# Performance work log

Measured on AMD Instinct MI355X. Metric: run time of the kernel, lower is better.

The kernel has to match this reference:

```python
import jax, jax.numpy as jnp
import numpy as np

B, T, D = 512, 128, 768
CD, SD, P = 192, 128, 128
FEAT = CD + SD + 1  # 321
LN_EPS = 1e-5


def setup_inputs() -> dict:
    key = jax.random.key(0)
    ks = jax.random.split(key, 10)
    return {
        'H': jax.random.normal(ks[0], (B, T, D), jnp.float32),
        'tt': jax.random.randint(ks[1], (B, T), 0, 2, jnp.int64),
        'attn': jnp.ones((B, T), jnp.int64),
        'Wc': jax.random.normal(ks[2], (CD, 2 * D), jnp.float32) * 0.02,
        'bc': jax.random.normal(ks[3], (CD,), jnp.float32) * 0.02,
        'Ws': jax.random.normal(ks[4], (SD, 2 * D), jnp.float32) * 0.02,
        'bs': jax.random.normal(ks[5], (SD,), jnp.float32) * 0.02,
        'gate': jnp.array([0.5], jnp.float32),
        'ln_g': jnp.ones((FEAT,), jnp.float32),
        'ln_b': jnp.zeros((FEAT,), jnp.float32),
        'Wcls': jax.random.normal(ks[6], (2, FEAT), jnp.float32) * 0.02,
        'bcls': jax.random.normal(ks[7], (2,), jnp.float32) * 0.02,
        'dirs': jax.random.normal(ks[8], (P, D), jnp.float32),
    }


def reference(H, tt, attn, Wc, bc, Ws, bs, gate, ln_g, ln_b, Wcls, bcls, dirs):
    dt = H.dtype
    cls = H[:, 0]                                   # [B, D]
    mask0 = (tt == 0) & (attn == 1)                 # [B, T]
    mask1 = (tt == 1) & (attn == 1)

    def mmean(mask):
        mf = mask.astype(dt)
        s = jnp.einsum('btd,bt->bd', H, mf)
        cnt = jnp.maximum(mask.sum(1, keepdims=True), 1).astype(dt)
        return s / cnt

    rep = jnp.concatenate([cls, mmean(mask0) - mmean(mask1)], axis=1)  # [B, 2D]
    C = rep @ Wc.T + bc
    S = rep @ Ws.T + bs
    g = jax.nn.sigmoid(gate)                        # [1]
    fused = jnp.concatenate([C * (1 - g), S * g], axis=1)  # [B, CD+SD]

    # batched max-sliced W1: project, push masked tokens to +inf, sort along T
    dirs_n = dirs / jnp.linalg.norm(dirs, axis=1, keepdims=True)
    proj = jnp.einsum('btd,pd->btp', H, dirs_n)     # [B, T, P]
    inf = jnp.asarray(jnp.inf, dt)
    xp = jnp.sort(jnp.where(mask0[:, :, None], proj, inf), axis=1)
    yp = jnp.sort(jnp.where(mask1[:, :, None], proj, inf), axis=1)
    n0 = mask0.sum(1)
    n1 = mask1.sum(1)
    mm = jnp.minimum(n0, n1)                        # [B] ragged truncation length
    valid = (jnp.arange(T)[None, :] < mm[:, None])[:, :, None]  # [B, T, 1]
    xs = jnp.where(valid, xp, 0.0)
    ys = jnp.where(valid, yp, 0.0)
    diff = jnp.abs(xs - ys).sum(1) / jnp.maximum(mm, 1)[:, None].astype(dt)  # [B, P]
    d_ot = diff.max(1, keepdims=True)               # [B, 1]

    feat = jnp.concatenate([fused, d_ot], axis=1)   # [B, 321]
    mu = feat.mean(-1, keepdims=True)
    var = feat.var(-1, keepdims=True)
    normed = (feat - mu) / jnp.sqrt(var + LN_EPS) * ln_g + ln_b
    logits = normed @ Wcls.T + bcls                 # [B, 2]

    ortho = jnp.mean((Wc @ Ws.T) ** 2)
    return logits, ortho
```

## Files before the change

kernel.cpp:

```cpp
#include <hip/hip_runtime.h>
#include <hip/hip_bf16.h>

constexpr int B_ = 512;
constexpr int T_ = 128;
constexpr int D_ = 768;
constexpr int CD_ = 192;
constexpr int SD_ = 128;
constexpr int P_ = 128;
constexpr int FEAT_ = 321;
constexpr float LN_EPS_ = 1e-5f;

constexpr size_t REP_SZ   = (size_t)B_ * 2 * D_;
constexpr size_t DN16_FLT = (size_t)P_ * D_ / 2;

typedef __attribute__((ext_vector_type(8))) short short8;
typedef __attribute__((ext_vector_type(4))) float f32x4;

__device__ __forceinline__ unsigned short f2bf(float x) {
    unsigned u = __float_as_uint(x);
    return (unsigned short)((u + 0x7FFFu + ((u >> 16) & 1u)) >> 16);
}
__device__ __forceinline__ float bf2f(unsigned short h) {
    return __uint_as_float((unsigned)h << 16);
}

__global__ __launch_bounds__(256) void k_dirs(const float* __restrict__ dirs,
                                              unsigned short* __restrict__ dn16) {
    int p = blockIdx.x;
    int tid = threadIdx.x;
    float s = 0.f;
    for (int d = tid; d < D_; d += 256) {
        float v = dirs[(size_t)p * D_ + d];
        s = fmaf(v, v, s);
    }
    __shared__ float red[256];
    red[tid] = s;
    __syncthreads();
    for (int off = 128; off > 0; off >>= 1) {
        if (tid < off) red[tid] += red[tid + off];
        __syncthreads();
    }
    float inv = 1.0f / sqrtf(red[0]);
    for (int d = tid; d < D_; d += 256) {
        dn16[(size_t)p * D_ + d] = f2bf(dirs[(size_t)p * D_ + d] * inv);
    }
}

constexpr int NIT_ = 24;
constexpr int BUF_U16_ = 8192;
constexpr int HT_STR_ = 136;

__global__ __launch_bounds__(512, 2) void k_projsort(const float* __restrict__ H,
                                                     const int* __restrict__ tt,
                                                     const int* __restrict__ attn,
                                                     const unsigned short* __restrict__ dn16,
                                                     float* __restrict__ rep,
                                                     float* __restrict__ d_ot) {
    const int b = blockIdx.x;
    const int tid = threadIdx.x;

    __shared__ __align__(16) unsigned short stage[2 * BUF_U16_];
    __shared__ __align__(16) unsigned short Ht[32 * HT_STR_];
    __shared__ __align__(16) unsigned short proj16[T_ * 128];
    __shared__ __align__(16) unsigned short mask16[2 * T_];
    __shared__ float m0s[T_], m1s[T_];
    __shared__ unsigned char pos_s[T_];
    __shared__ int ncnt[2];
    __shared__ float dred[512];

    unsigned char* xb = (unsigned char*)stage;
    unsigned char* yb = xb + 64 * 128;

    const float* Hb = H + (size_t)b * T_ * D_;
    const int srow = tid >> 2;
    const int scp  = tid & 3;
    const int sclog = scp ^ ((srow >> 1) & 3);
    const float* gA = Hb + (size_t)srow * D_ + sclog * 8;
    const unsigned short* gB = dn16 + (size_t)srow * D_ + sclog * 8;
    const int dOff = srow * 32 + scp * 8;

    float4 a0A = *reinterpret_cast<const float4*>(gA);
    float4 a1A = *reinterpret_cast<const float4*>(gA + 4);
    short8 bvA = *reinterpret_cast<const short8*>(gB);
    float4 a0B = *reinterpret_cast<const float4*>(gA + 32);
    float4 a1B = *reinterpret_cast<const float4*>(gA + 36);
    short8 bvB = *reinterpret_cast<const short8*>(gB + 32);

    if (tid < 2) ncnt[tid] = 0;
    __syncthreads();
    if (tid < T_) {
        int t = tt[b * T_ + tid];
        int a = attn[b * T_ + tid];
        float m0 = (t == 0 && a == 1) ? 1.f : 0.f;
        float m1 = (t == 1 && a == 1) ? 1.f : 0.f;
        m0s[tid] = m0;
        m1s[tid] = m1;
        mask16[tid] = (m0 > 0.f) ? 0x3F80u : 0u;
        mask16[T_ + tid] = (m1 > 0.f) ? 0x3F80u : 0u;
        if (m0 > 0.f) atomicAdd(&ncnt[0], 1);
        if (m1 > 0.f) atomicAdd(&ncnt[1], 1);
    }
    __syncthreads();
    const int n0 = ncnt[0], n1 = ncnt[1];
    const int ntot = n0 + n1;
    const float inv0 = 1.f / (float)max(n0, 1);
    const float inv1 = 1.f / (float)max(n1, 1);
    if (tid < T_) {
        float me0 = m0s[tid], me1 = m1s[tid];
        unsigned char pp = 0xFF;
        if (me0 > 0.f || me1 > 0.f) {
            bool g1 = (me1 > 0.f);
            const float* ms = g1 ? m1s : m0s;
            int pos = g1 ? n0 : 0;
            for (int j = 0; j < tid; ++j) pos += (ms[j] > 0.f) ? 1 : 0;
            pp = (unsigned char)pos;
        }
        pos_s[tid] = pp;
    }
    __syncthreads();

    const int wv = tid >> 6;
    const int wr = wv >> 2;
    const int wc = wv & 3;
    const int lane = tid & 63;
    const int fr = lane & 15;
    const int kg = lane >> 4;
    const int fk = kg * 8;
    const int ck = (kg ^ ((fr >> 1) & 3)) * 8;
    const int baseA = (64 * wr + fr) * 32 + ck;
    const int baseB = 4096 + (32 * wc + 16 * 0 + fr) * 32 + ck;
    const bool repw = (wv >= 6);
    const int jf = wv & 1;
    float* repb = rep + (size_t)b * 2 * D_;

    f32x4 acc[4][2];
#pragma unroll
    for (int m = 0; m < 4; ++m)
#pragma unroll
        for (int n = 0; n < 2; ++n) acc[m][n] = (f32x4){0.f, 0.f, 0.f, 0.f};

    auto body = [&](int it, unsigned short* sb, float4& pa0, float4& pa1, short8& pbv) {
        short8 w;
        w[0] = (short)f2bf(pa0.x); w[1] = (short)f2bf(pa0.y);
        w[2] = (short)f2bf(pa0.z); w[3] = (short)f2bf(pa0.w);
        w[4] = (short)f2bf(pa1.x); w[5] = (short)f2bf(pa1.y);
        w[6] = (short)f2bf(pa1.z); w[7] = (short)f2bf(pa1.w);
        *reinterpret_cast<short8*>(sb + dOff) = w;
        *reinterpret_cast<short8*>(sb + 4096 + dOff) = pbv;
#pragma unroll
        for (int j = 0; j < 8; ++j)
            Ht[(sclog * 8 + j) * HT_STR_ + srow] = (unsigned short)w[j];
        if (srow == 0) {
            *reinterpret_cast<float4*>(repb + it * 32 + sclog * 8) = pa0;
            *reinterpret_cast<float4*>(repb + it * 32 + sclog * 8 + 4) = pa1;
        }
        if (it + 2 < NIT_) {
            pa0 = *reinterpret_cast<const float4*>(gA + (it + 2) * 32);
            pa1 = *reinterpret_cast<const float4*>(gA + (it + 2) * 32 + 4);
            pbv = *reinterpret_cast<const short8*>(gB + (it + 2) * 32);
        }
        asm volatile("s_waitcnt lgkmcnt(0)" ::: "memory");
        __builtin_amdgcn_s_barrier();
        asm volatile("" ::: "memory");

        short8 af[4], bf_[2];
#pragma unroll
        for (int m = 0; m < 4; ++m)
            af[m] = *reinterpret_cast<const short8*>(sb + baseA + 512 * m);
#pragma unroll
        for (int n = 0; n < 2; ++n)
            bf_[n] = *reinterpret_cast<const short8*>(sb + baseB + 512 * n);
#pragma unroll
        for (int m = 0; m < 4; ++m)
#pragma unroll
            for (int n = 0; n < 2; ++n)
                acc[m][n] = __builtin_amdgcn_mfma_f32_16x16x32_bf16(af[m], bf_[n], acc[m][n], 0, 0, 0);

        if (repw) {
            f32x4 ar = (f32x4){0.f, 0.f, 0.f, 0.f};
#pragma unroll
            for (int tc = 0; tc < 4; ++tc) {
                short8 am = {0, 0, 0, 0, 0, 0, 0, 0};
                if (fr < 2) am = *reinterpret_cast<const short8*>(&mask16[fr * T_ + tc * 32 + fk]);
                short8 bm = *reinterpret_cast<const short8*>(&Ht[(16 * jf + fr) * HT_STR_ + tc * 32 + fk]);
                ar = __builtin_amdgcn_mfma_f32_16x16x32_bf16(am, bm, ar, 0, 0, 0);
            }
            if (lane < 16) repb[D_ + it * 32 + jf * 16 + lane] = ar[0] * inv0 - ar[1] * inv1;
        }
        asm volatile("" ::: "memory");
        __builtin_amdgcn_s_barrier();
        asm volatile("" ::: "memory");
    };

    for (int i2 = 0; i2 < NIT_ / 2; ++i2) {
        body(2 * i2,     stage,            a0A, a1A, bvA);
        body(2 * i2 + 1, stage + BUF_U16_, a0B, a1B, bvB);
    }

#pragma unroll
    for (int m = 0; m < 4; ++m) {
        int row0 = 64 * wr + 16 * m + kg * 4;
#pragma unroll
        for (int r = 0; r < 4; ++r) {
            int pp = pos_s[row0 + r];
            if (pp != 0xFF) {
#pragma unroll
                for (int n = 0; n < 2; ++n) {
                    int col = 32 * wc + 16 * n + fr;
                    unsigned bb = f2bf(acc[m][n][r]);
                    unsigned su = bb ^ ((bb >> 15) ? 0xFFFFu : 0x8000u);
                    proj16[pp * 128 + col] = (unsigned short)su;
                }
            }
        }
    }
    __syncthreads();

    const int mmv = min(n0, n1);
    const int c = tid & 127;
    const int q = tid >> 7;
#pragma unroll
    for (int pass = 0; pass < 2; ++pass) {
        const int pbase = q * 32 + pass * 16;
        unsigned kv[16];
        int cnt[16];
#pragma unroll
        for (int ii = 0; ii < 16; ++ii) {
            int p = pbase + ii;
            unsigned key = 0xFFFFFFFFu;
            if (p < ntot) {
                unsigned su = proj16[p * 128 + c];
                key = ((unsigned)(p >= n0) << 31) | (su << 8) | (unsigned)p;
            }
            kv[ii] = key;
            cnt[ii] = 0;
        }
        int lo, hi;
        if (pbase + 16 <= n0) { lo = 0;  hi = n0;   }
        else if (pbase >= n0) { lo = n0; hi = ntot; }
        else                  { lo = 0;  hi = ntot; }
        for (int j = lo; j < hi; ++j) {
            unsigned su = proj16[j * 128 + c];
            unsigned kw = ((unsigned)(j >= n0) << 31) | (su << 8) | (unsigned)j;
#pragma unroll
            for (int ii = 0; ii < 16; ++ii) cnt[ii] += (kw < kv[ii]) ? 1 : 0;
        }
#pragma unroll
        for (int ii = 0; ii < 16; ++ii) {
            int p = pbase + ii;
            if (p < ntot) {
                int rank = cnt[ii] - ((p >= n0 && lo == 0) ? n0 : 0);
                if (rank < mmv) {
                    unsigned char* buf = (p >= n0) ? yb : xb;
                    buf[rank * 128 + c] = (unsigned char)p;
                }
            }
        }
    }
    __syncthreads();

    float part = 0.f;
    for (int r = q; r < mmv; r += 4) {
        unsigned sx = proj16[(int)xb[r * 128 + c] * 128 + c];
        unsigned sy = proj16[(int)yb[r * 128 + c] * 128 + c];
        unsigned bx = sx ^ ((sx >> 15) ? 0x8000u : 0xFFFFu);
        unsigned by = sy ^ ((sy >> 15) ? 0x8000u : 0xFFFFu);
        part += fabsf(bf2f((unsigned short)bx) - bf2f((unsigned short)by));
    }
    dred[tid] = part;
    __syncthreads();
    if (tid < 128) {
        float invm = 1.f / (float)max(mmv, 1);
        dred[tid] = (dred[tid] + dred[tid + 128] + dred[tid + 256] + dred[tid + 384]) * invm;
    }
    __syncthreads();
    if (tid < 64) {
        float m = fmaxf(dred[tid], dred[tid + 64]);
#pragma unroll
        for (int off = 32; off > 0; off >>= 1) m = fmaxf(m, __shfl_xor(m, off));
        if (tid == 0) d_ot[b] = m;
    }
}

__global__ __launch_bounds__(320) void k_head(const float* __restrict__ rep,
                                              const float* __restrict__ Wc,
                                              const float* __restrict__ bc,
                                              const float* __restrict__ Ws,
                                              const float* __restrict__ bs,
                                              const float* __restrict__ gate,
                                              const float* __restrict__ lng,
                                              const float* __restrict__ lnb,
                                              const float* __restrict__ Wcls,
                                              const float* __restrict__ bcls,
                                              const float* __restrict__ d_ot,
                                              float* __restrict__ out) {
    int b0 = blockIdx.x * 4;
    int tid = threadIdx.x;
    __shared__ __align__(16) float repS[4 * 1536];
    __shared__ float featS[4 * FEAT_];

    const float4* repg = reinterpret_cast<const float4*>(rep + (size_t)b0 * 1536);
    float4* repl = reinterpret_cast<float4*>(repS);
    for (int i = tid; i < 1536; i += 320) repl[i] = repg[i];
    __syncthreads();

    float g = 1.f / (1.f + expf(-gate[0]));

    {
        int o = tid;
        bool isC = o < CD_;
        const float* w = isC ? (Wc + (size_t)o * 1536) : (Ws + (size_t)(o - CD_) * 1536);
        float bias = isC ? bc[o] : bs[o - CD_];
        float scale = isC ? (1.f - g) : g;
        const float4* w4 = reinterpret_cast<const float4*>(w);
        float a0 = 0.f, a1 = 0.f, a2 = 0.f, a3 = 0.f;
        for (int k4 = 0; k4 < 384; ++k4) {
            float4 wv = w4[k4];
            float4 r0 = repl[k4];
            float4 r1 = repl[384 + k4];
            float4 r2 = repl[768 + k4];
            float4 r3 = repl[1152 + k4];
            a0 += fmaf(wv.x, r0.x, fmaf(wv.y, r0.y, fmaf(wv.z, r0.z, wv.w * r0.w)));
            a1 += fmaf(wv.x, r1.x, fmaf(wv.y, r1.y, fmaf(wv.z, r1.z, wv.w * r1.w)));
            a2 += fmaf(wv.x, r2.x, fmaf(wv.y, r2.y, fmaf(wv.z, r2.z, wv.w * r2.w)));
            a3 += fmaf(wv.x, r3.x, fmaf(wv.y, r3.y, fmaf(wv.z, r3.z, wv.w * r3.w)));
        }
        featS[0 * FEAT_ + o] = (a0 + bias) * scale;
        featS[1 * FEAT_ + o] = (a1 + bias) * scale;
        featS[2 * FEAT_ + o] = (a2 + bias) * scale;
        featS[3 * FEAT_ + o] = (a3 + bias) * scale;
    }
    if (tid < 4) featS[tid * FEAT_ + 320] = d_ot[b0 + tid];
    __syncthreads();

    int w = tid >> 6, lane = tid & 63;
    if (w < 4) {
        const float* f = featS + w * FEAT_;
        float s = 0.f, s2 = 0.f;
        for (int i = lane; i < FEAT_; i += 64) {
            float v = f[i];
            s += v;
            s2 = fmaf(v, v, s2);
        }
#pragma unroll
        for (int off = 32; off > 0; off >>= 1) {
            s += __shfl_xor(s, off);
            s2 += __shfl_xor(s2, off);
        }
        float mu = s * (1.f / (float)FEAT_);
        float var = fmaxf(s2 * (1.f / (float)FEAT_) - mu * mu, 0.f);
        float rstd = 1.0f / sqrtf(var + LN_EPS_);
        float l0 = 0.f, l1 = 0.f;
        for (int i = lane; i < FEAT_; i += 64) {
            float nv = (f[i] - mu) * rstd * lng[i] + lnb[i];
            l0 = fmaf(nv, Wcls[i], l0);
            l1 = fmaf(nv, Wcls[FEAT_ + i], l1);
        }
#pragma unroll
        for (int off = 32; off > 0; off >>= 1) {
            l0 += __shfl_xor(l0, off);
            l1 += __shfl_xor(l1, off);
        }
        if (lane == 0) {
            out[(size_t)(b0 + w) * 2 + 0] = l0 + bcls[0];
            out[(size_t)(b0 + w) * 2 + 1] = l1 + bcls[1];
        }
    }
}

__global__ __launch_bounds__(256) void k_ortho(const float* __restrict__ Wc,
                                               const float* __restrict__ Ws,
                                               float* __restrict__ part) {
    int i = blockIdx.x;
    int tid = threadIdx.x;
    __shared__ float wrow[1536];
    __shared__ float tmp[256];
    for (int k = tid; k < 1536; k += 256) wrow[k] = Wc[(size_t)i * 1536 + k];
    __syncthreads();
    int j = tid & 127, h = tid >> 7;
    const float* wsr = Ws + (size_t)j * 1536 + h * 768;
    const float* wr = wrow + h * 768;
    float s = 0.f;
    for (int k = 0; k < 768; ++k) s = fmaf(wr[k], wsr[k], s);
    tmp[tid] = s;
    __syncthreads();
    if (tid < 128) {
        float d = tmp[tid] + tmp[tid + 128];
        tmp[tid] = d * d;
    }
    __syncthreads();
    for (int off = 64; off > 0; off >>= 1) {
        if (tid < off) tmp[tid] += tmp[tid + off];
        __syncthreads();
    }
    if (tid == 0) part[i] = tmp[0];
}

__global__ __launch_bounds__(256) void k_ortho2(const float* __restrict__ part,
                                                float* __restrict__ out) {
    int tid = threadIdx.x;
    __shared__ float red[256];
    red[tid] = (tid < CD_) ? part[tid] : 0.f;
    __syncthreads();
    for (int off = 128; off > 0; off >>= 1) {
        if (tid < off) red[tid] += red[tid + off];
        __syncthreads();
    }
    if (tid == 0) out[(size_t)B_ * 2] = red[0] / (float)(CD_ * SD_);
}

extern "C" void kernel_launch(void* const* d_in, const int* in_sizes, int n_in,
                              void* d_out, int out_size, void* d_ws, size_t ws_size,
                              hipStream_t stream) {
    const float* H    = (const float*)d_in[0];
    const int*   tt   = (const int*)d_in[1];
    const int*   attn = (const int*)d_in[2];
    const float* Wc   = (const float*)d_in[3];
    const float* bc   = (const float*)d_in[4];
    const float* Ws   = (const float*)d_in[5];
    const float* bs   = (const float*)d_in[6];
    const float* gate = (const float*)d_in[7];
    const float* lng  = (const float*)d_in[8];
    const float* lnb  = (const float*)d_in[9];
    const float* Wcls = (const float*)d_in[10];
    const float* bcls = (const float*)d_in[11];
    const float* dirs = (const float*)d_in[12];

    float* ws    = (float*)d_ws;
    float* rep   = ws;
    unsigned short* dn16 = (unsigned short*)(ws + REP_SZ);
    float* dot   = ws + REP_SZ + DN16_FLT;
    float* part  = dot + B_;
    float* out   = (float*)d_out;

    k_dirs<<<P_, 256, 0, stream>>>(dirs, dn16);
    k_projsort<<<B_, 512, 0, stream>>>(H, tt, attn, dn16, rep, dot);
    k_head<<<B_ / 4, 320, 0, stream>>>(rep, Wc, bc, Ws, bs, gate, lng, lnb, Wcls, bcls, dot, out);
    k_ortho<<<CD_, 256, 0, stream>>>(Wc, Ws, part);
    k_ortho2<<<1, 256, 0, stream>>>(part, out);
}
```

Before: 191.3 us.

## Load MFMA operands straight from global memory and compute masked means with shuffles

The projection-sort kernel stops staging H and directions through double-buffered LDS with barriers. Each wave now loads its MFMA fragments directly from global memory. Masks and token positions are built with wave ballots and popcounts instead of shared-memory atomics and serial prefix loops. The masked means are computed in fp32 by wave 0-3 shuffle reductions into a scratch area reused from proj16, and the rank sort handles 32 keys per thread in a single pass. This removes per-iteration barriers and LDS traffic but repeats global/L2 reads of dn16 in every block, drops the min-2-blocks occupancy hint, and adds register pressure.

```diff
diff --git a/kernel.cpp b/kernel.cpp
--- a/kernel.cpp
+++ b/kernel.cpp
@@ -15,6 +15,7 @@
 
 typedef __attribute__((ext_vector_type(8))) short short8;
 typedef __attribute__((ext_vector_type(4))) float f32x4;
+typedef unsigned long long ull_t;
 
 __device__ __forceinline__ unsigned short f2bf(float x) {
     unsigned u = __float_as_uint(x);
@@ -47,90 +48,65 @@
 }
 
 constexpr int NIT_ = 24;
-constexpr int BUF_U16_ = 8192;
-constexpr int HT_STR_ = 136;
-
-__global__ __launch_bounds__(512, 2) void k_projsort(const float* __restrict__ H,
-                                                     const int* __restrict__ tt,
-                                                     const int* __restrict__ attn,
-                                                     const unsigned short* __restrict__ dn16,
-                                                     float* __restrict__ rep,
-                                                     float* __restrict__ d_ot) {
+
+__global__ __launch_bounds__(512) void k_projfull(const float* __restrict__ H,
+                                                  const int* __restrict__ tt,
+                                                  const int* __restrict__ attn,
+                                                  const unsigned short* __restrict__ dn16,
+                                                  float* __restrict__ rep,
+                                                  float* __restrict__ d_ot) {
     const int b = blockIdx.x;
     const int tid = threadIdx.x;
-
-    __shared__ __align__(16) unsigned short stage[2 * BUF_U16_];
-    __shared__ __align__(16) unsigned short Ht[32 * HT_STR_];
-    __shared__ __align__(16) unsigned short proj16[T_ * 128];
-    __shared__ __align__(16) unsigned short mask16[2 * T_];
-    __shared__ float m0s[T_], m1s[T_];
+    const int lane = tid & 63;
+    const int w = tid >> 6;
+    const int wp = w >> 2;
+    const int wt = w & 3;
+    const int fr = lane & 15;
+    const int kg = lane >> 4;
+
+    __shared__ __align__(16) unsigned short proj16[128 * 128];
+    __shared__ unsigned char xb[64 * 128];
+    __shared__ unsigned char yb[64 * 128];
+    __shared__ float dred[512];
     __shared__ unsigned char pos_s[T_];
-    __shared__ int ncnt[2];
-    __shared__ float dred[512];
-
-    unsigned char* xb = (unsigned char*)stage;
-    unsigned char* yb = xb + 64 * 128;
-
-    const float* Hb = H + (size_t)b * T_ * D_;
-    const int srow = tid >> 2;
-    const int scp  = tid & 3;
-    const int sclog = scp ^ ((srow >> 1) & 3);
-    const float* gA = Hb + (size_t)srow * D_ + sclog * 8;
-    const unsigned short* gB = dn16 + (size_t)srow * D_ + sclog * 8;
-    const int dOff = srow * 32 + scp * 8;
-
-    float4 a0A = *reinterpret_cast<const float4*>(gA);
-    float4 a1A = *reinterpret_cast<const float4*>(gA + 4);
-    short8 bvA = *reinterpret_cast<const short8*>(gB);
-    float4 a0B = *reinterpret_cast<const float4*>(gA + 32);
-    float4 a1B = *reinterpret_cast<const float4*>(gA + 36);
-    short8 bvB = *reinterpret_cast<const short8*>(gB + 32);
-
-    if (tid < 2) ncnt[tid] = 0;
-    __syncthreads();
-    if (tid < T_) {
-        int t = tt[b * T_ + tid];
-        int a = attn[b * T_ + tid];
-        float m0 = (t == 0 && a == 1) ? 1.f : 0.f;
-        float m1 = (t == 1 && a == 1) ? 1.f : 0.f;
-        m0s[tid] = m0;
-        m1s[tid] = m1;
-        mask16[tid] = (m0 > 0.f) ? 0x3F80u : 0u;
-        mask16[T_ + tid] = (m1 > 0.f) ? 0x3F80u : 0u;
-        if (m0 > 0.f) atomicAdd(&ncnt[0], 1);
-        if (m1 > 0.f) atomicAdd(&ncnt[1], 1);
-    }
-    __syncthreads();
-    const int n0 = ncnt[0], n1 = ncnt[1];
+    float* repP = (float*)proj16;
+
+    const int myt = 64 * wp + lane;
+    int vt = tt[b * T_ + myt];
+    int va = attn[b * T_ + myt];
+    bool m0 = (vt == 0) && (va == 1);
+    bool m1 = (vt == 1) && (va == 1);
+    ull_t bal0 = __ballot(m0);
+    ull_t bal1 = __ballot(m1);
+    ull_t* xch = (ull_t*)dred;
+    if (lane == 0 && (w == 0 || w == 4)) {
+        xch[wp * 2] = bal0;
+        xch[wp * 2 + 1] = bal1;
+    }
+    __syncthreads();
+    const ull_t lo0 = xch[0], lo1 = xch[1], hi0 = xch[2], hi1 = xch[3];
+    const int n0 = __popcll(lo0) + __popcll(hi0);
+    const int n1 = __popcll(lo1) + __popcll(hi1);
     const int ntot = n0 + n1;
     const float inv0 = 1.f / (float)max(n0, 1);
     const float inv1 = 1.f / (float)max(n1, 1);
-    if (tid < T_) {
-        float me0 = m0s[tid], me1 = m1s[tid];
-        unsigned char pp = 0xFF;
-        if (me0 > 0.f || me1 > 0.f) {
-            bool g1 = (me1 > 0.f);
-            const float* ms = g1 ? m1s : m0s;
-            int pos = g1 ? n0 : 0;
-            for (int j = 0; j < tid; ++j) pos += (ms[j] > 0.f) ? 1 : 0;
-            pp = (unsigned char)pos;
-        }
-        pos_s[tid] = pp;
-    }
-    __syncthreads();
-
-    const int wv = tid >> 6;
-    const int wr = wv >> 2;
-    const int wc = wv & 3;
-    const int lane = tid & 63;
-    const int fr = lane & 15;
-    const int kg = lane >> 4;
-    const int fk = kg * 8;
-    const int ck = (kg ^ ((fr >> 1) & 3)) * 8;
-    const int baseA = (64 * wr + fr) * 32 + ck;
-    const int baseB = 4096 + (32 * wc + 16 * 0 + fr) * 32 + ck;
-    const bool repw = (wv >= 6);
-    const int jf = wv & 1;
+    ull_t below = (1ull << lane) - 1ull;
+    int mypos = 0xFF;
+    if (m0) mypos = (wp ? __popcll(lo0) : 0) + __popcll((wp ? hi0 : lo0) & below);
+    else if (m1) mypos = n0 + (wp ? __popcll(lo1) : 0) + __popcll((wp ? hi1 : lo1) & below);
+    if (w == 0 || w == 4) pos_s[myt] = (unsigned char)mypos;
+
+    const int t0 = 32 * wt + fr;
+    const int t1 = t0 + 16;
+    const float fm00 = (float)(((t0 < 64 ? lo0 >> t0 : hi0 >> (t0 - 64))) & 1ull);
+    const float fm01 = (float)(((t1 < 64 ? lo0 >> t1 : hi0 >> (t1 - 64))) & 1ull);
+    const float fm10 = (float)(((t0 < 64 ? lo1 >> t0 : hi1 >> (t0 - 64))) & 1ull);
+    const float fm11 = (float)(((t1 < 64 ? lo1 >> t1 : hi1 >> (t1 - 64))) & 1ull);
+
+    const float* Hb = H + (size_t)b * T_ * D_;
+    const float* gB0 = Hb + (size_t)t0 * D_ + kg * 8;
+    const float* gB1 = Hb + (size_t)t1 * D_ + kg * 8;
+    const unsigned short* gA = dn16 + (size_t)(64 * wp + fr) * D_ + kg * 8;
     float* repb = rep + (size_t)b * 2 * D_;
 
     f32x4 acc[4][2];
@@ -139,78 +115,93 @@
 #pragma unroll
         for (int n = 0; n < 2; ++n) acc[m][n] = (f32x4){0.f, 0.f, 0.f, 0.f};
 
-    auto body = [&](int it, unsigned short* sb, float4& pa0, float4& pa1, short8& pbv) {
-        short8 w;
-        w[0] = (short)f2bf(pa0.x); w[1] = (short)f2bf(pa0.y);
-        w[2] = (short)f2bf(pa0.z); w[3] = (short)f2bf(pa0.w);
-        w[4] = (short)f2bf(pa1.x); w[5] = (short)f2bf(pa1.y);
-        w[6] = (short)f2bf(pa1.z); w[7] = (short)f2bf(pa1.w);
-        *reinterpret_cast<short8*>(sb + dOff) = w;
-        *reinterpret_cast<short8*>(sb + 4096 + dOff) = pbv;
-#pragma unroll
-        for (int j = 0; j < 8; ++j)
-            Ht[(sclog * 8 + j) * HT_STR_ + srow] = (unsigned short)w[j];
-        if (srow == 0) {
-            *reinterpret_cast<float4*>(repb + it * 32 + sclog * 8) = pa0;
-            *reinterpret_cast<float4*>(repb + it * 32 + sclog * 8 + 4) = pa1;
-        }
-        if (it + 2 < NIT_) {
-            pa0 = *reinterpret_cast<const float4*>(gA + (it + 2) * 32);
-            pa1 = *reinterpret_cast<const float4*>(gA + (it + 2) * 32 + 4);
-            pbv = *reinterpret_cast<const short8*>(gB + (it + 2) * 32);
-        }
-        asm volatile("s_waitcnt lgkmcnt(0)" ::: "memory");
-        __builtin_amdgcn_s_barrier();
-        asm volatile("" ::: "memory");
-
-        short8 af[4], bf_[2];
-#pragma unroll
-        for (int m = 0; m < 4; ++m)
-            af[m] = *reinterpret_cast<const short8*>(sb + baseA + 512 * m);
-#pragma unroll
-        for (int n = 0; n < 2; ++n)
-            bf_[n] = *reinterpret_cast<const short8*>(sb + baseB + 512 * n);
-#pragma unroll
-        for (int m = 0; m < 4; ++m)
-#pragma unroll
-            for (int n = 0; n < 2; ++n)
-                acc[m][n] = __builtin_amdgcn_mfma_f32_16x16x32_bf16(af[m], bf_[n], acc[m][n], 0, 0, 0);
-
-        if (repw) {
-            f32x4 ar = (f32x4){0.f, 0.f, 0.f, 0.f};
-#pragma unroll
-            for (int tc = 0; tc < 4; ++tc) {
-                short8 am = {0, 0, 0, 0, 0, 0, 0, 0};
-                if (fr < 2) am = *reinterpret_cast<const short8*>(&mask16[fr * T_ + tc * 32 + fk]);
-                short8 bm = *reinterpret_cast<const short8*>(&Ht[(16 * jf + fr) * HT_STR_ + tc * 32 + fk]);
-                ar = __builtin_amdgcn_mfma_f32_16x16x32_bf16(am, bm, ar, 0, 0, 0);
-            }
-            if (lane < 16) repb[D_ + it * 32 + jf * 16 + lane] = ar[0] * inv0 - ar[1] * inv1;
-        }
-        asm volatile("" ::: "memory");
-        __builtin_amdgcn_s_barrier();
-        asm volatile("" ::: "memory");
-    };
-
-    for (int i2 = 0; i2 < NIT_ / 2; ++i2) {
-        body(2 * i2,     stage,            a0A, a1A, bvA);
-        body(2 * i2 + 1, stage + BUF_U16_, a0B, a1B, bvB);
-    }
-
+    for (int it = 0; it < NIT_; ++it) {
+        const int k0 = it * 32;
+        short8 a0 = *reinterpret_cast<const short8*>(gA + k0);
+        short8 a1 = *reinterpret_cast<const short8*>(gA + 16 * D_ + k0);
+        short8 a2 = *reinterpret_cast<const short8*>(gA + 32 * D_ + k0);
+        short8 a3 = *reinterpret_cast<const short8*>(gA + 48 * D_ + k0);
+        float4 h00 = *reinterpret_cast<const float4*>(gB0 + k0);
+        float4 h01 = *reinterpret_cast<const float4*>(gB0 + k0 + 4);
+        float4 h10 = *reinterpret_cast<const float4*>(gB1 + k0);
+        float4 h11 = *reinterpret_cast<const float4*>(gB1 + k0 + 4);
+
+        if (wp == 0) {
+            float p0[8], p1[8];
+            float h0v[8] = {h00.x, h00.y, h00.z, h00.w, h01.x, h01.y, h01.z, h01.w};
+            float h1v[8] = {h10.x, h10.y, h10.z, h10.w, h11.x, h11.y, h11.z, h11.w};
+#pragma unroll
+            for (int j = 0; j < 8; ++j) {
+                p0[j] = h0v[j] * fm00 + h1v[j] * fm01;
+                p1[j] = h0v[j] * fm10 + h1v[j] * fm11;
+            }
+#pragma unroll
+            for (int off = 1; off < 16; off <<= 1) {
+#pragma unroll
+                for (int j = 0; j < 8; ++j) {
+                    p0[j] += __shfl_xor(p0[j], off);
+                    p1[j] += __shfl_xor(p1[j], off);
+                }
+            }
+            if (fr == 0) {
+                float* dst = repP + (it * 4 + wt) * 64 + kg * 16;
+                *reinterpret_cast<float4*>(dst)      = (float4){p0[0], p1[0], p0[1], p1[1]};
+                *reinterpret_cast<float4*>(dst + 4)  = (float4){p0[2], p1[2], p0[3], p1[3]};
+                *reinterpret_cast<float4*>(dst + 8)  = (float4){p0[4], p1[4], p0[5], p1[5]};
+                *reinterpret_cast<float4*>(dst + 12) = (float4){p0[6], p1[6], p0[7], p1[7]};
+            }
+        }
+
+        short8 b0, b1;
+        b0[0] = (short)f2bf(h00.x); b0[1] = (short)f2bf(h00.y);
+        b0[2] = (short)f2bf(h00.z); b0[3] = (short)f2bf(h00.w);
+        b0[4] = (short)f2bf(h01.x); b0[5] = (short)f2bf(h01.y);
+        b0[6] = (short)f2bf(h01.z); b0[7] = (short)f2bf(h01.w);
+        b1[0] = (short)f2bf(h10.x); b1[1] = (short)f2bf(h10.y);
+        b1[2] = (short)f2bf(h10.z); b1[3] = (short)f2bf(h10.w);
+        b1[4] = (short)f2bf(h11.x); b1[5] = (short)f2bf(h11.y);
+        b1[6] = (short)f2bf(h11.z); b1[7] = (short)f2bf(h11.w);
+
+        acc[0][0] = __builtin_amdgcn_mfma_f32_16x16x32_bf16(a0, b0, acc[0][0], 0, 0, 0);
+        acc[0][1] = __builtin_amdgcn_mfma_f32_16x16x32_bf16(a0, b1, acc[0][1], 0, 0, 0);
+        acc[1][0] = __builtin_amdgcn_mfma_f32_16x16x32_bf16(a1, b0, acc[1][0], 0, 0, 0);
+        acc[1][1] = __builtin_amdgcn_mfma_f32_16x16x32_bf16(a1, b1, acc[1][1], 0, 0, 0);
+        acc[2][0] = __builtin_amdgcn_mfma_f32_16x16x32_bf16(a2, b0, acc[2][0], 0, 0, 0);
+        acc[2][1] = __builtin_amdgcn_mfma_f32_16x16x32_bf16(a2, b1, acc[2][1], 0, 0, 0);
+        acc[3][0] = __builtin_amdgcn_mfma_f32_16x16x32_bf16(a3, b0, acc[3][0], 0, 0, 0);
+        acc[3][1] = __builtin_amdgcn_mfma_f32_16x16x32_bf16(a3, b1, acc[3][1], 0, 0, 0);
+    }
+    __syncthreads();
+
+    for (int i = tid; i < D_; i += 512) {
+        int k0i = i >> 5, dl = i & 31;
+        const float* src = repP + (k0i * 4) * 64 + dl * 2;
+        float s0 = src[0] + src[64] + src[128] + src[192];
+        float s1 = src[1] + src[65] + src[129] + src[193];
+        repb[D_ + i] = s0 * inv0 - s1 * inv1;
+    }
+    if (tid < 192) {
+        float4 v = *reinterpret_cast<const float4*>(Hb + tid * 4);
+        *reinterpret_cast<float4*>(repb + tid * 4) = v;
+    }
+    __syncthreads();
+
+    const int pp0 = pos_s[t0];
+    const int pp1 = pos_s[t1];
 #pragma unroll
     for (int m = 0; m < 4; ++m) {
-        int row0 = 64 * wr + 16 * m + kg * 4;
+        int prow = 64 * wp + 16 * m + kg * 4;
 #pragma unroll
         for (int r = 0; r < 4; ++r) {
-            int pp = pos_s[row0 + r];
-            if (pp != 0xFF) {
-#pragma unroll
-                for (int n = 0; n < 2; ++n) {
-                    int col = 32 * wc + 16 * n + fr;
-                    unsigned bb = f2bf(acc[m][n][r]);
-                    unsigned su = bb ^ ((bb >> 15) ? 0xFFFFu : 0x8000u);
-                    proj16[pp * 128 + col] = (unsigned short)su;
-                }
+            if (pp0 != 0xFF) {
+                unsigned bb = f2bf(acc[m][0][r]);
+                unsigned su = bb ^ ((bb >> 15) ? 0xFFFFu : 0x8000u);
+                proj16[pp0 * 128 + prow + r] = (unsigned short)su;
+            }
+            if (pp1 != 0xFF) {
+                unsigned bb = f2bf(acc[m][1][r]);
+                unsigned su = bb ^ ((bb >> 15) ? 0xFFFFu : 0x8000u);
+                proj16[pp1 * 128 + prow + r] = (unsigned short)su;
             }
         }
     }
@@ -219,13 +210,12 @@
     const int mmv = min(n0, n1);
     const int c = tid & 127;
     const int q = tid >> 7;
-#pragma unroll
-    for (int pass = 0; pass < 2; ++pass) {
-        const int pbase = q * 32 + pass * 16;
-        unsigned kv[16];
-        int cnt[16];
-#pragma unroll
-        for (int ii = 0; ii < 16; ++ii) {
+    const int pbase = q * 32;
+    {
+        unsigned kv[32];
+        int cnt[32];
+#pragma unroll
+        for (int ii = 0; ii < 32; ++ii) {
             int p = pbase + ii;
             unsigned key = 0xFFFFFFFFu;
             if (p < ntot) {
@@ -236,17 +226,17 @@
             cnt[ii] = 0;
         }
         int lo, hi;
-        if (pbase + 16 <= n0) { lo = 0;  hi = n0;   }
+        if (pbase + 32 <= n0) { lo = 0;  hi = n0;   }
         else if (pbase >= n0) { lo = n0; hi = ntot; }
         else                  { lo = 0;  hi = ntot; }
         for (int j = lo; j < hi; ++j) {
             unsigned su = proj16[j * 128 + c];
             unsigned kw = ((unsigned)(j >= n0) << 31) | (su << 8) | (unsigned)j;
 #pragma unroll
-            for (int ii = 0; ii < 16; ++ii) cnt[ii] += (kw < kv[ii]) ? 1 : 0;
-        }
-#pragma unroll
-        for (int ii = 0; ii < 16; ++ii) {
+            for (int ii = 0; ii < 32; ++ii) cnt[ii] += (kw < kv[ii]) ? 1 : 0;
+        }
+#pragma unroll
+        for (int ii = 0; ii < 32; ++ii) {
             int p = pbase + ii;
             if (p < ntot) {
                 int rank = cnt[ii] - ((p >= n0 && lo == 0) ? n0 : 0);
@@ -264,8 +254,8 @@
         unsigned sx = proj16[(int)xb[r * 128 + c] * 128 + c];
         unsigned sy = proj16[(int)yb[r * 128 + c] * 128 + c];
         unsigned bx = sx ^ ((sx >> 15) ? 0x8000u : 0xFFFFu);
-        unsigned by = sy ^ ((sy >> 15) ? 0x8000u : 0xFFFFu);
-        part += fabsf(bf2f((unsigned short)bx) - bf2f((unsigned short)by));
+        unsigned byv = sy ^ ((sy >> 15) ? 0x8000u : 0xFFFFu);
+        part += fabsf(bf2f((unsigned short)bx) - bf2f((unsigned short)byv));
     }
     dred[tid] = part;
     __syncthreads();
@@ -434,7 +424,7 @@
     float* out   = (float*)d_out;
 
     k_dirs<<<P_, 256, 0, stream>>>(dirs, dn16);
-    k_projsort<<<B_, 512, 0, stream>>>(H, tt, attn, dn16, rep, dot);
+    k_projfull<<<B_, 512, 0, stream>>>(H, tt, attn, dn16, rep, dot);
     k_head<<<B_ / 4, 320, 0, stream>>>(rep, Wc, bc, Ws, bs, gate, lng, lnb, Wcls, bcls, dot, out);
     k_ortho<<<CD_, 256, 0, stream>>>(Wc, Ws, part);
     k_ortho2<<<1, 256, 0, stream>>>(part, out);
```

Result: slower. 240.9 us (+25.9%).
